# Optimization experiments

Hardware: AMD Instinct MI355X
Metric: run time of the kernel (lower is better)

## Reference

```python
import jax, jax.numpy as jnp
import numpy as np

SE = 128        # num_sensors
T = 256         # timesteps
D_OB = 4        # d_ob_emb
D_PE = 16
D_STATIC = 64
B = 128
N_HEADS = 4
D_FF = 128
N_TRAN = 2
N_PROP = 2
N_CLASSES = 2
D_FEAT = T * D_OB              # 1024, prop-layer feature dim
D_MODEL = SE * D_OB + D_PE     # 528, transformer d_model
D_FINAL = D_MODEL + SE * D_OB  # 1040, mlp input (with static emb)
LN_EPS = 1e-5
NEG_INF = -1e9


def _layernorm(x, g, b):
    m = jnp.mean(x, axis=-1, keepdims=True)
    v = jnp.mean(jnp.square(x - m), axis=-1, keepdims=True)
    return (x - m) * jax.lax.rsqrt(v + LN_EPS) * g + b


def setup_inputs() -> dict:
    key = jax.random.key(0)
    ks = iter(jax.random.split(key, 40))

    def g(shape, scale=0.02):
        return jax.random.normal(next(ks), shape, jnp.float32) * scale

    a = float(np.sqrt(6.0 / (1 + SE * D_OB)))  # glorot for R_u
    inp = {
        'src': jax.random.normal(next(ks), (T, B, 2 * SE), jnp.float32),
        'times': jax.random.uniform(next(ks), (T, B), jnp.float32) * T,
        'lengths': jax.random.randint(next(ks), (B,), 1, T + 1),
        'static': jax.random.normal(next(ks), (B, D_STATIC), jnp.float32),
        'R_u': jax.random.uniform(next(ks), (1, SE * D_OB), jnp.float32, -a, a),
        'static_W': g((SE * D_OB, D_STATIC)),
        'static_b': g((SE * D_OB,)),
        'p_Wq': g((N_PROP, D_FEAT, D_FEAT)),
        'p_Wk': g((N_PROP, D_FEAT, D_FEAT)),
        'p_Wv': g((N_PROP, D_FEAT, D_FEAT)),
        'p_bq': g((N_PROP, D_FEAT)),
        'p_bk': g((N_PROP, D_FEAT)),
        'p_bv': g((N_PROP, D_FEAT)),
        'p_Wskip': g((N_PROP, D_FEAT, D_FEAT)),
        'p_bskip': g((N_PROP, D_FEAT)),
        't_Wqkv': g((N_TRAN, 3 * D_MODEL, D_MODEL)),
        't_bqkv': g((N_TRAN, 3 * D_MODEL)),
        't_Wo': g((N_TRAN, D_MODEL, D_MODEL)),
        't_bo': g((N_TRAN, D_MODEL)),
        't_W1': g((N_TRAN, D_FF, D_MODEL)),
        't_b1': g((N_TRAN, D_FF)),
        't_W2': g((N_TRAN, D_MODEL, D_FF)),
        't_b2': g((N_TRAN, D_MODEL)),
        't_ln1g': jnp.ones((N_TRAN, D_MODEL), jnp.float32),
        't_ln1b': jnp.zeros((N_TRAN, D_MODEL), jnp.float32),
        't_ln2g': jnp.ones((N_TRAN, D_MODEL), jnp.float32),
        't_ln2b': jnp.zeros((N_TRAN, D_MODEL), jnp.float32),
        'mlp_W1': g((D_FINAL, D_FINAL)),
        'mlp_b1': g((D_FINAL,)),
        'mlp_W2': g((N_CLASSES, D_FINAL)),
        'mlp_b2': g((N_CLASSES,)),
    }
    return inp


def reference(src, times, lengths, static, R_u, static_W, static_b,
              p_Wq, p_Wk, p_Wv, p_bq, p_bk, p_bv, p_Wskip, p_bskip,
              t_Wqkv, t_bqkv, t_Wo, t_bo, t_W1, t_b1, t_W2, t_b2,
              t_ln1g, t_ln1b, t_ln2g, t_ln2b,
              mlp_W1, mlp_b1, mlp_W2, mlp_b2):
    # --- positional encoding (PositionalEncodingTF): sin/cos of times over timescales ---
    ts = jnp.asarray(float(T)) ** jnp.linspace(0.0, 1.0, D_PE // 2)
    st = times[..., None] / ts                       # (T,B,D_PE//2)
    pe = jnp.concatenate([jnp.sin(st), jnp.cos(st)], axis=-1)  # (T,B,D_PE)

    static_emb = static @ static_W.T + static_b      # (B, SE*D_OB)

    # --- per-sensor observation embedding ---
    x = src[:, :, :SE]
    x = jnp.repeat(x, D_OB, axis=-1)                 # (T,B,SE*D_OB)
    h = jax.nn.relu(x * R_u)                         # dropout = identity (eval)

    # --- diagonalized graphs: each batch element is a fully-connected Se-node graph.
    # The block-diagonal edge list over B*Se*Se edges is equivalent to dense
    # batched attention (B, Se, Se); we honor that structure densely. ---
    hg = h.reshape(T, B, SE, D_OB).transpose(1, 2, 0, 3).reshape(B, SE, D_FEAT)
    W = jnp.ones((B, SE, SE), h.dtype)               # edge weights [b, tgt, src], adj=ones
    scale = 1.0 / jnp.sqrt(jnp.asarray(D_FEAT, h.dtype))
    for l in range(N_PROP):
        q = hg @ p_Wq[l].T + p_bq[l]
        k = hg @ p_Wk[l].T + p_bk[l]
        v = hg @ p_Wv[l].T + p_bv[l]
        scores = jnp.einsum('bid,bjd->bij', q, k) * scale   # i=target, j=source
        alpha = jax.nn.softmax(scores, axis=-1)              # softmax over sources
        hg = jnp.einsum('bij,bjd->bid', alpha * W, v) + hg @ p_Wskip[l].T + p_bskip[l]
        W = alpha                                            # attn weights feed next layer

    out = hg.reshape(B, SE, T, D_OB).transpose(2, 0, 1, 3).reshape(T, B, SE * D_OB)
    out = jnp.concatenate([out, pe], axis=2)          # (T,B,D_MODEL)

    # --- transformer encoder (post-norm, relu FF, key_padding_mask) ---
    time_mask = jnp.arange(T)[None, :] >= lengths[:, None]   # (B,T) True = pad
    hd = D_MODEL // N_HEADS
    xx = out
    for l in range(N_TRAN):
        qkv = xx @ t_Wqkv[l].T + t_bqkv[l]            # (T,B,3*D_MODEL)
        q, k, v = jnp.split(qkv, 3, axis=-1)
        def _heads(z):
            return z.reshape(T, B, N_HEADS, hd).transpose(1, 2, 0, 3)  # (B,H,T,hd)
        qh, kh, vh = _heads(q), _heads(k), _heads(v)
        att = jnp.einsum('bhqd,bhkd->bhqk', qh, kh) / jnp.sqrt(jnp.asarray(hd, xx.dtype))
        att = jnp.where(time_mask[:, None, None, :], NEG_INF, att)
        att = jax.nn.softmax(att, axis=-1)
        o = jnp.einsum('bhqk,bhkd->bhqd', att, vh).transpose(2, 0, 1, 3).reshape(T, B, D_MODEL)
        o = o @ t_Wo[l].T + t_bo[l]
        xx = _layernorm(xx + o, t_ln1g[l], t_ln1b[l])
        ff = jax.nn.relu(xx @ t_W1[l].T + t_b1[l]) @ t_W2[l].T + t_b2[l]
        xx = _layernorm(xx + ff, t_ln2g[l], t_ln2b[l])

    # --- masked mean pooling over time, static concat, MLP head ---
    keep = (~time_mask).astype(xx.dtype).T[:, :, None]        # (T,B,1)
    pooled = jnp.sum(xx * keep, axis=0) / (lengths[:, None].astype(xx.dtype) + 1.0)
    pooled = jnp.concatenate([pooled, static_emb], axis=1)    # (B, D_FINAL)
    hid = jax.nn.relu(pooled @ mlp_W1.T + mlp_b1)
    return hid @ mlp_W2.T + mlp_b2                            # (B, N_CLASSES)
```

## Files before the change

### kernel.cpp

```cpp
#include <hip/hip_runtime.h>
#include <hip/hip_bf16.h>
#include <math.h>

#define SE_    128
#define T_     256
#define B_     128
#define NH_    4
#define HD_    132
#define D_MODEL_ 528
#define D_FINAL_ 1040
#define D_FF_  128

typedef __hip_bfloat16 bf16;
typedef __attribute__((ext_vector_type(8))) short bf16x8v;
typedef __attribute__((ext_vector_type(4))) float f32x4;

__device__ __forceinline__ float bfb(unsigned short u){
  union { float f; unsigned int i; } c; c.i = ((unsigned int)u) << 16; return c.f;
}
__device__ __forceinline__ unsigned short bfr(float x){
  unsigned u = __builtin_bit_cast(unsigned, x);
  unsigned r = (u + 0x7FFFu + ((u >> 16) & 1u)) >> 16;
  return (unsigned short)r;
}
__device__ __forceinline__ void split1(float x, short& h, short& l){
  const unsigned short hu = bfr(x);
  const unsigned short lu = bfr(x - bfb(hu));
  h = (short)hu; l = (short)lu;
}
__device__ __forceinline__ float prd(const short* p, long i, long lo){
  return bfb((unsigned short)p[i]) + bfb((unsigned short)p[i+lo]);
}
__device__ __forceinline__ float rdIn(const void* p, long i, int f32){
  return f32 ? ((const float*)p)[i] : __bfloat162float(((const bf16*)p)[i]);
}

__global__ void detect_k(const void* __restrict__ src, int* __restrict__ flag){
  const unsigned int* p = (const unsigned int*)src;
  int bad = 0;
  for (int i = threadIdx.x; i < 4096; i += 256){
    const unsigned int lo = p[i] & 0xFFFFu;
    const unsigned int e = (lo >> 7) & 0xFFu;
    if (e >= 0xC0u) bad++;
  }
  __shared__ int red[256];
  red[threadIdx.x] = bad; __syncthreads();
  for (int h = 128; h > 0; h >>= 1){
    if (threadIdx.x < h) red[threadIdx.x] += red[threadIdx.x+h];
    __syncthreads();
  }
  if (threadIdx.x == 0) *flag = (red[0] > 64) ? 1 : 0;
}

#define MAXE 40
struct CvtTab {
  const void* src[MAXE];
  long srcOff[MAXE];
  long dstOff[MAXE];
  int n[MAXE];
  int bstart[MAXE];
  int cnt;
};
__global__ void cvt_all(CvtTab tb, short* __restrict__ wts, long loW, const int* __restrict__ flag){
  const int b = blockIdx.x;
  int e = 0;
  for (int i = 1; i < tb.cnt; ++i) if (tb.bstart[i] <= b) e = i;
  const long i = (long)(b - tb.bstart[e])*256 + threadIdx.x;
  if (i >= tb.n[e]) return;
  const float v = rdIn(tb.src[e], tb.srcOff[e] + i, *flag);
  short h, l; split1(v, h, l);
  wts[tb.dstOff[e] + i] = h;
  wts[tb.dstOff[e] + i + loW] = l;
}

__device__ __forceinline__ int swz(int r){ return (r&3) ^ ((r>>2)&3); }

__device__ __forceinline__ void gllstage_pair(const short* __restrict__ g, long lo, long ld,
    int kb, int row_g0, int rmax, int tid, short* Lh, short* Ll){
  const int w = tid>>6, ln = tid&63;
  #pragma unroll
  for (int inst=0; inst<2; ++inst){
    const int r = (w*2+inst)*16 + (ln>>2);
    int gr = row_g0 + r; if (gr > rmax) gr = rmax;
    const int q = (ln&3) ^ (((ln>>2)&3) ^ ((ln>>4)&3));
    const short* p = g + (long)gr*ld + kb + q*8;
    short* dh = Lh + (w*2+inst)*512;
    short* dl = Ll + (w*2+inst)*512;
    __builtin_amdgcn_global_load_lds(
        (const __attribute__((address_space(1))) void*)p,
        (__attribute__((address_space(3))) void*)dh, 16, 0, 0);
    __builtin_amdgcn_global_load_lds(
        (const __attribute__((address_space(1))) void*)(p + lo),
        (__attribute__((address_space(3))) void*)dl, 16, 0, 0);
  }
}

__device__ __forceinline__ void regstage_pair(const short* __restrict__ g, long lo, long ld,
    int kb, int K, int row_g0, int rmax, int tid, short* Lh, short* Ll){
  const int r = tid>>1;
  int gr = row_g0 + r; if (gr > rmax) gr = rmax;
  const int s = swz(r);
  #pragma unroll
  for (int cq=0;cq<2;++cq){
    const int q = (tid&1)*2 + cq;
    const int k0 = kb + q*8;
    short bh[8], bl[8];
    const short* p = g + (long)gr*ld + k0;
    if (k0 + 8 <= K){
      *(int2*)(bh)   = *(const int2*)(p);      *(int2*)(bh+4) = *(const int2*)(p+4);
      *(int2*)(bl)   = *(const int2*)(p+lo);   *(int2*)(bl+4) = *(const int2*)(p+lo+4);
    } else {
      #pragma unroll
      for (int e=0;e<8;++e){
        const bool ok = (k0+e) < K;
        bh[e] = ok ? p[e] : (short)0;
        bl[e] = ok ? p[lo+e] : (short)0;
      }
    }
    const int c = q ^ s;
    *(int4*)&Lh[r*32 + c*8] = *(const int4*)bh;
    *(int4*)&Ll[r*32 + c*8] = *(const int4*)bl;
  }
}

__device__ __forceinline__ void regstage_f32(const float* __restrict__ g, long ld,
    int kb, int K, int row_g0, int rmax, int tid, short* Lh, short* Ll){
  const int r = tid>>1;
  int gr = row_g0 + r; if (gr > rmax) gr = rmax;
  const int s = swz(r);
  #pragma unroll
  for (int cq=0;cq<2;++cq){
    const int q = (tid&1)*2 + cq;
    const int k0 = kb + q*8;
    short bh[8], bl[8];
    const float* p = g + (long)gr*ld + k0;
    if (k0 + 8 <= K){
      float f[8];
      *(float4*)(f)   = *(const float4*)(p);
      *(float4*)(f+4) = *(const float4*)(p+4);
      #pragma unroll
      for (int e=0;e<8;++e) split1(f[e], bh[e], bl[e]);
    } else {
      #pragma unroll
      for (int e=0;e<8;++e){
        const float v = (k0+e < K) ? p[e] : 0.f;
        split1(v, bh[e], bl[e]);
      }
    }
    const int c = q ^ s;
    *(int4*)&Lh[r*32 + c*8] = *(const int4*)bh;
    *(int4*)&Ll[r*32 + c*8] = *(const int4*)bl;
  }
}

__device__ __forceinline__ void rd_frags(const short* Lh, const short* Ll,
                                         int wbase, int fr, int qlog,
                                         bf16x8v ah[4], bf16x8v al[4]){
  const int cs = (qlog ^ ((fr&3) ^ ((fr>>2)&3))) * 8;
  #pragma unroll
  for (int i=0;i<4;++i){
    const int r_ = wbase + i*16 + fr;
    ah[i] = *reinterpret_cast<const bf16x8v*>(&Lh[r_*32 + cs]);
    al[i] = *reinterpret_cast<const bf16x8v*>(&Ll[r_*32 + cs]);
  }
}

struct Route { short* C; long ldc; long lo; long sC; long sC2; int nEnd; int fl; };

template<bool SPLITA, bool GLL>
__global__ __launch_bounds__(256, 2) void gemm_s(
    const void* __restrict__ Ag, long loA,
    const short* __restrict__ Bg, long loB,
    const short* __restrict__ bias, long loBias,
    int M, int N, int K, long lda, long ldb,
    int nz1, long sA, long sB, long sA2, long sB2,
    int relu, int nroute, Route r0, Route r1, Route r2, float mult)
{
  __shared__ short As_h[128*32], As_l[128*32], Bs_h[128*32], Bs_l[128*32];
  const int tid = threadIdx.x;
  const int z1 = blockIdx.z % nz1, z2 = blockIdx.z / nz1;
  const int m0 = blockIdx.y*128, n0 = blockIdx.x*128;
  const void* A;
  if (SPLITA) A = (const void*)((const float*)Ag + z1*sA + z2*sA2);
  else        A = (const void*)((const short*)Ag + z1*sA + z2*sA2);
  const short* B = Bg + z1*sB + z2*sB2;
  short* Cb0 = r0.C + z1*r0.sC + z2*r0.sC2;
  short* Cb1 = (nroute > 1) ? (r1.C + z1*r1.sC + z2*r1.sC2) : nullptr;
  short* Cb2 = (nroute > 2) ? (r2.C + z1*r2.sC + z2*r2.sC2) : nullptr;

  const int lane = tid & 63, wv = tid >> 6;
  const int wm = (wv >> 1)*64, wn = (wv & 1)*64;
  const int fr = lane & 15, qlog = lane >> 4;

  f32x4 acc[4][4] = {};
  for (int kb = 0; kb < K; kb += 32){
    const bool tail = (kb + 32 > K);
    if (SPLITA) regstage_f32((const float*)A, lda, kb, K, m0, M-1, tid, As_h, As_l);
    else if (GLL && !tail) gllstage_pair((const short*)A, loA, lda, kb, m0, M-1, tid, As_h, As_l);
    else regstage_pair((const short*)A, loA, lda, kb, K, m0, M-1, tid, As_h, As_l);
    if (GLL && !tail) gllstage_pair(B, loB, ldb, kb, n0, N-1, tid, Bs_h, Bs_l);
    else regstage_pair(B, loB, ldb, kb, K, n0, N-1, tid, Bs_h, Bs_l);
    __syncthreads();

    bf16x8v ah[4], al[4], bh[4], bl[4];
    rd_frags(As_h, As_l, wm, fr, qlog, ah, al);
    rd_frags(Bs_h, Bs_l, wn, fr, qlog, bh, bl);
    #pragma unroll
    for (int j=0;j<4;++j)
      #pragma unroll
      for (int i=0;i<4;++i){
        acc[i][j] = __builtin_amdgcn_mfma_f32_16x16x32_bf16(ah[i], bh[j], acc[i][j], 0,0,0);
        acc[i][j] = __builtin_amdgcn_mfma_f32_16x16x32_bf16(ah[i], bl[j], acc[i][j], 0,0,0);
        acc[i][j] = __builtin_amdgcn_mfma_f32_16x16x32_bf16(al[i], bh[j], acc[i][j], 0,0,0);
      }
    __syncthreads();
  }

  const int cr = (lane >> 4)*4, cc = lane & 15;
  #pragma unroll
  for (int i=0;i<4;++i){
    #pragma unroll
    for (int j=0;j<4;++j){
      #pragma unroll
      for (int rr=0;rr<4;++rr){
        const int gm = m0 + wm + i*16 + cr + rr;
        const int gn = n0 + wn + j*16 + cc;
        if (gm < M && gn < N){
          float v = acc[i][j][rr] * mult;
          if (bias) v += prd(bias, gn, loBias);
          if (relu) v = fmaxf(v, 0.f);
          short* Cp; long ldc, lo; int fl, cn;
          if (nroute > 1 && gn >= r0.nEnd){
            if (nroute > 2 && gn >= r1.nEnd){ Cp=Cb2; ldc=r2.ldc; lo=r2.lo; fl=r2.fl; cn=gn-r1.nEnd; }
            else                            { Cp=Cb1; ldc=r1.ldc; lo=r1.lo; fl=r1.fl; cn=gn-r0.nEnd; }
          } else                            { Cp=Cb0; ldc=r0.ldc; lo=r0.lo; fl=r0.fl; cn=gn; }
          const long idx = (fl & 1) ? ((long)cn*ldc + gm) : ((long)gm*ldc + cn);
          if (fl & 2) v += prd(Cp, idx, lo);
          short h, l; split1(v, h, l);
          Cp[idx] = h; Cp[idx + lo] = l;
        }
      }
    }
  }
}

template<int NN, bool GLL>
__global__ __launch_bounds__(256, 2) void gemm_sm(
    const short* __restrict__ Ag, long loA, const short* __restrict__ Bg, long loB,
    int K, long lda, long ldb,
    int nz1, long sA, long sB, long sA2, long sB2,
    float* __restrict__ Sg, long sS, long sS2, int ldS,
    float mult, const int* __restrict__ lengths, int b0,
    const float* __restrict__ mulP, long sMul)
{
  __shared__ short As_h[128*32], As_l[128*32], Bs_h[128*32], Bs_l[128*32];
  const int tid = threadIdx.x;
  const int z1 = blockIdx.z % nz1, z2 = blockIdx.z / nz1;
  const int m0 = blockIdx.y*128;
  const short* A = Ag + z1*sA + z2*sA2;
  const short* B = Bg + z1*sB + z2*sB2;
  float* S = Sg + z1*sS + z2*sS2;

  const int lane = tid & 63, wv = tid >> 6;
  const int wm = (wv >> 1)*64, wn = (wv & 1)*64;
  const int fr = lane & 15, qlog = lane >> 4;
  const int cr = (lane >> 4)*4, cc = lane & 15;

  for (int nh = 0; nh < NN; nh += 128){
    f32x4 acc[4][4] = {};
    for (int kb = 0; kb < K; kb += 32){
      const bool tail = (kb + 32 > K);
      if (GLL && !tail){
        gllstage_pair(A, loA, lda, kb, m0, m0+127, tid, As_h, As_l);
        gllstage_pair(B, loB, ldb, kb, nh, nh+127, tid, Bs_h, Bs_l);
      } else {
        regstage_pair(A, loA, lda, kb, K, m0, m0+127, tid, As_h, As_l);
        regstage_pair(B, loB, ldb, kb, K, nh, nh+127, tid, Bs_h, Bs_l);
      }
      __syncthreads();
      bf16x8v ah[4], al[4], bh[4], bl[4];
      rd_frags(As_h, As_l, wm, fr, qlog, ah, al);
      rd_frags(Bs_h, Bs_l, wn, fr, qlog, bh, bl);
      #pragma unroll
      for (int j=0;j<4;++j)
        #pragma unroll
        for (int i=0;i<4;++i){
          acc[i][j] = __builtin_amdgcn_mfma_f32_16x16x32_bf16(ah[i], bh[j], acc[i][j], 0,0,0);
          acc[i][j] = __builtin_amdgcn_mfma_f32_16x16x32_bf16(ah[i], bl[j], acc[i][j], 0,0,0);
          acc[i][j] = __builtin_amdgcn_mfma_f32_16x16x32_bf16(al[i], bh[j], acc[i][j], 0,0,0);
        }
      __syncthreads();
    }
    #pragma unroll
    for (int i=0;i<4;++i)
      #pragma unroll
      for (int j=0;j<4;++j)
        #pragma unroll
        for (int rr=0;rr<4;++rr){
          const int gm = m0 + wm + i*16 + cr + rr;
          const int gn = nh + wn + j*16 + cc;
          S[(long)gm*ldS + gn] = acc[i][j][rr] * mult;
        }
  }
  __syncthreads();

  constexpr int CH = NN / 64;
  const int cbase = lane*CH;
  int lim = NN;
  if (lengths){ const int L = lengths[b0 + z1]; lim = (L < NN) ? L : NN; }

  float v[CH], vn[CH], mcur[CH], mnxt[CH];
  {
    float* row0 = S + (long)(m0 + wv*32)*ldS + cbase;
    #pragma unroll
    for (int e=0;e<CH;++e) v[e] = row0[e];
    if (mulP){
      const float* mr = mulP + z1*sMul + (long)(m0 + wv*32)*ldS + cbase;
      #pragma unroll
      for (int e=0;e<CH;++e) mcur[e] = mr[e];
    }
  }
  for (int i = 0; i < 32; ++i){
    if (i < 31){
      float* rn = S + (long)(m0 + wv*32 + i + 1)*ldS + cbase;
      #pragma unroll
      for (int e=0;e<CH;++e) vn[e] = rn[e];
      if (mulP){
        const float* mr = mulP + z1*sMul + (long)(m0 + wv*32 + i + 1)*ldS + cbase;
        #pragma unroll
        for (int e=0;e<CH;++e) mnxt[e] = mr[e];
      }
    }
    float mx = -3.0e38f;
    #pragma unroll
    for (int e=0;e<CH;++e) if (cbase+e < lim) mx = fmaxf(mx, v[e]);
    #pragma unroll
    for (int o=32;o>0;o>>=1) mx = fmaxf(mx, __shfl_xor(mx, o, 64));
    float sm = 0.f;
    #pragma unroll
    for (int e=0;e<CH;++e){
      v[e] = (cbase+e < lim) ? __expf(v[e] - mx) : 0.f;
      sm += v[e];
    }
    #pragma unroll
    for (int o=32;o>0;o>>=1) sm += __shfl_xor(sm, o, 64);
    const float inv = 1.f / sm;
    float* row = S + (long)(m0 + wv*32 + i)*ldS + cbase;
    if (mulP){
      #pragma unroll
      for (int e=0;e<CH;++e) row[e] = v[e]*inv*mcur[e];
    } else {
      #pragma unroll
      for (int e=0;e<CH;++e) row[e] = v[e]*inv;
    }
    #pragma unroll
    for (int e=0;e<CH;++e){ v[e] = vn[e]; mcur[e] = mnxt[e]; }
  }
}

__global__ void build_hg(const void* __restrict__ src, const short* __restrict__ Ru, long loW,
                         short* __restrict__ hg, long loH, const int* __restrict__ flag, int b0){
  const int t = blockIdx.x, bl = blockIdx.y, se = threadIdx.x;
  const int f32 = *flag;
  const float s = rdIn(src, ((long)t*B_ + (b0+bl))*(2*SE_) + se, f32);
  const long o = ((long)bl*SE_ + se)*1024 + t*4;
  #pragma unroll
  for (int j=0;j<4;++j){
    const float v = fmaxf(s * prd(Ru, se*4+j, loW), 0.f);
    short h, l; split1(v, h, l);
    hg[o+j] = h; hg[o+j+loH] = l;
  }
}

__global__ void build_xx(const short* __restrict__ hg, long loH,
                         const short* __restrict__ times, long loW,
                         short* __restrict__ xx, long loX, int b0, int G){
  const int blk = blockIdx.x;
  const int t = blk / G, bl = blk % G, b = b0 + bl;
  const int tid = threadIdx.x;
  const float tm = prd(times, (long)t*B_ + b, loW);
  for (int c = tid; c < D_MODEL_; c += 256){
    float v;
    if (c < SE_*4){
      v = prd(hg, ((long)bl*SE_ + (c>>2))*1024 + t*4 + (c&3), loH);
    } else {
      const int p = c - SE_*4;
      const int i = p & 7;
      const float ts = exp2f(8.0f * (float)i / 7.0f);
      const float st = tm / ts;
      v = (p < 8) ? sinf(st) : cosf(st);
    }
    short h, l; split1(v, h, l);
    const long o = ((long)t*B_ + b)*D_MODEL_ + c;
    xx[o] = h; xx[o+loX] = l;
  }
}

__device__ __forceinline__ void ln_body_p(short* px, long loX, const short* pr, long loR,
                                          const short* g, const short* bb, long loW, int tid){
  const float x0 = prd(px,tid,loX)     + prd(pr,tid,loR);
  const float x1 = prd(px,tid+256,loX) + prd(pr,tid+256,loR);
  const float x2 = (tid < 16) ? (prd(px,tid+512,loX) + prd(pr,tid+512,loR)) : 0.f;
  __shared__ float rs[256], rq[256];
  rs[tid] = x0 + x1 + x2;
  rq[tid] = x0*x0 + x1*x1 + x2*x2;
  __syncthreads();
  for (int h = 128; h > 0; h >>= 1){
    if (tid < h){ rs[tid] += rs[tid+h]; rq[tid] += rq[tid+h]; }
    __syncthreads();
  }
  const float mean = rs[0] * (1.0f/528.0f);
  const float var  = rq[0] * (1.0f/528.0f) - mean*mean;
  const float inv = rsqrtf(var + 1e-5f);
  short h, l;
  split1((x0-mean)*inv*prd(g,tid,loW) + prd(bb,tid,loW), h, l);
  px[tid] = h; px[tid+loX] = l;
  split1((x1-mean)*inv*prd(g,tid+256,loW) + prd(bb,tid+256,loW), h, l);
  px[tid+256] = h; px[tid+256+loX] = l;
  if (tid < 16){
    split1((x2-mean)*inv*prd(g,tid+512,loW) + prd(bb,tid+512,loW), h, l);
    px[tid+512] = h; px[tid+512+loX] = l;
  }
}

__global__ __launch_bounds__(256) void ln_res_attn(short* __restrict__ xx, long loX,
    const short* __restrict__ res, long loR,
    const short* __restrict__ g, const short* __restrict__ bb, long loW, int b0){
  const int z = blockIdx.x >> 8, t = blockIdx.x & 255;
  short* px = xx + ((long)t*B_ + b0 + z)*D_MODEL_;
  const short* pr = res + (long)blockIdx.x*D_MODEL_;
  ln_body_p(px, loX, pr, loR, g, bb, loW, threadIdx.x);
}

__global__ __launch_bounds__(256) void ln_res_rows(short* __restrict__ xx, long loX,
    const short* __restrict__ res, long loR,
    const short* __restrict__ g, const short* __restrict__ bb, long loW, int r0){
  short* px = xx + ((long)r0 + blockIdx.x)*D_MODEL_;
  const short* pr = res + (long)blockIdx.x*D_MODEL_;
  ln_body_p(px, loX, pr, loR, g, bb, loW, threadIdx.x);
}

__global__ void pool_k(const short* __restrict__ xx, long loX, const int* __restrict__ len,
                       short* __restrict__ pooled, long loP){
  const int b = blockIdx.y;
  const int c = blockIdx.x*256 + threadIdx.x;
  if (c >= D_MODEL_) return;
  const int L = len[b];
  float s = 0.f;
  for (int t = 0; t < L; ++t) s += prd(xx, ((long)t*B_ + b)*D_MODEL_ + c, loX);
  short h, l; split1(s / (float)(L + 1), h, l);
  pooled[(long)b*D_FINAL_ + c] = h;
  pooled[(long)b*D_FINAL_ + c + loP] = l;
}

__global__ void logits_k(const short* __restrict__ hid, long loH,
                         const short* __restrict__ W2, const short* __restrict__ b2, long loW,
                         void* __restrict__ out, const int* __restrict__ flag){
  const int z = blockIdx.x;
  const int b = z >> 1, c = z & 1;
  const int lane = threadIdx.x;
  float s = 0.f;
  for (int k = lane; k < D_FINAL_; k += 64)
    s += prd(hid, (long)b*D_FINAL_ + k, loH) * prd(W2, (long)c*D_FINAL_ + k, loW);
  #pragma unroll
  for (int o = 32; o > 0; o >>= 1) s += __shfl_down(s, o, 64);
  if (lane == 0){
    const float r = s + prd(b2, c, loW);
    if (*flag) ((float*)out)[z] = r;
    else       ((bf16*)out)[z] = __float2bfloat16(r);
  }
}

extern "C" void kernel_launch(void* const* d_in, const int* in_sizes, int n_in,
                              void* d_out, int out_size, void* d_ws, size_t ws_size,
                              hipStream_t stream) {
  const int* lengths = (const int*)d_in[2];
  char* ws = (char*)d_ws;
  const size_t KB = 1024;

  short* wtsH = (short*)ws;
  int* flag = (int*)(ws + 47500*KB);
  short* xxH = (short*)(ws + 48000*KB);
  const long loXX = 17301504;
  char* SC = ws + 115600*KB;

  short* hgA = (short*)(SC + 0*KB);      const long loHG = 2097152;
  short* hgB = (short*)(SC + 8192*KB);
  short* qkc = (short*)(SC + 16384*KB);  const long loQK1 = 4194304;
  short* VtS = (short*)(SC + 32768*KB);  const long loVT1 = 2097152;
  float* S0c = (float*)(SC + 40960*KB);
  float* S1c = (float*)(SC + 41984*KB);
  short* qkb = (short*)(SC + 0*KB);      const long loQK2 = 4325376;
  short* o_c = (short*)(SC + 0*KB);      const long loOC  = 2162688;
  short* pjb = (short*)(SC + 8448*KB);   const long loPJ  = 2162688;
  short* vtb = (short*)(SC + 16896*KB);  const long loVT2 = 2162688;
  float* att = (float*)(SC + 25344*KB);
  short* ff1 = (short*)(SC + 0*KB);      const long loFF  = 4194304;
  short* pj2 = (short*)(SC + 16896*KB);  const long loPJ2 = 4325376;
  short* pooled = (short*)(SC + 0*KB);   const long loPO  = 133120;
  short* hid    = (short*)(SC + 1024*KB);

  CvtTab tb; long cur = 0; int nb = 0; int e = 0;
  auto add = [&](int idx, long so, long n)->long{
    tb.src[e] = d_in[idx]; tb.srcOff[e] = so; tb.dstOff[e] = cur;
    tb.n[e] = (int)n; tb.bstart[e] = nb;
    nb += (int)((n + 255)/256); cur += n; e++;
    return cur - n;
  };
  const long oT  = add(1,0,32768);
  const long oSt = add(3,0,8192);
  const long oRu = add(4,0,512);
  const long oSW = add(5,0,32768);
  const long oSb = add(6,0,512);
  long oQKSV[2], oBQ[2];
  for (int l = 0; l < 2; ++l){
    oQKSV[l] = add(7, (long)l*1048576, 1048576);
    add(8,  (long)l*1048576, 1048576);
    add(13, (long)l*1048576, 1048576);
    add(9,  (long)l*1048576, 1048576);
  }
  for (int l = 0; l < 2; ++l){
    oBQ[l] = add(10, (long)l*1024, 1024);
    add(11, (long)l*1024, 1024);
    add(14, (long)l*1024, 1024);
    add(12, (long)l*1024, 1024);
  }
  const long oWqkv = add(15,0,1672704);
  const long obqkv = add(16,0,3168);
  const long oWo = add(17,0,557568);
  const long obo = add(18,0,1056);
  const long oW1 = add(19,0,135168);
  const long ob1 = add(20,0,256);
  const long oW2 = add(21,0,135168);
  const long ob2 = add(22,0,1056);
  const long og1 = add(23,0,1056);
  const long obb1 = add(24,0,1056);
  const long og2 = add(25,0,1056);
  const long obb2 = add(26,0,1056);
  const long oM1 = add(27,0,1081600);
  const long oM1b = add(28,0,1040);
  const long oM2 = add(29,0,2080);
  const long oM2b = add(30,0,2);
  tb.cnt = e;
  const long loW = (cur + 7) & ~7L;

  detect_k<<<1,256,0,stream>>>(d_in[0], flag);
  cvt_all<<<nb,256,0,stream>>>(tb, wtsH, loW, flag);

  const Route RZ{nullptr,0,0,0,0,0,0};

  const int G1 = 16;
  for (int b0 = 0; b0 < B_; b0 += G1){
    build_hg<<<dim3(T_, G1), 128, 0, stream>>>(d_in[0], wtsH+oRu, loW, hgA, loHG, flag, b0);
    short* curb = hgA; short* nxtb = hgB;
    for (int l = 0; l < 2; ++l){
      float* S = (l == 0) ? S0c : S1c;
      {
        Route q{qkc, 2048, loQK1, 0, 0, 2048, 0};
        Route s{nxtb, 1024, loHG, 0, 0, 3072, 0};
        Route v{VtS, 2048, loVT1, 0, 0, 4096, 1};
        gemm_s<false,true><<<dim3(32,16,1),256,0,stream>>>(
            curb, loHG, wtsH+oQKSV[l], loW, wtsH+oBQ[l], loW,
            2048, 4096, 1024, 1024, 1024,
            1, 0,0,0,0, 0, 3, q, s, v, 1.f);
      }
      gemm_sm<128,true><<<dim3(1,1,G1),256,0,stream>>>(
          qkc, loQK1, qkc+1024, loQK1,
          1024, 2048, 2048,
          G1, 262144, 262144, 0, 0,
          S, 16384, 0, 128,
          0.03125f, nullptr, 0,
          (l == 1) ? S0c : nullptr, 16384);
      {
        Route c{nxtb, 1024, loHG, 131072, 0, 1024, 2};
        gemm_s<true,true><<<dim3(8,1,G1),256,0,stream>>>(
            S, 0, VtS, loVT1, nullptr, 0,
            128, 1024, 128, 128, 2048,
            G1, 16384, 128, 0, 0, 0, 1, c, RZ, RZ, 1.f);
      }
      short* t_ = curb; curb = nxtb; nxtb = t_;
    }
    build_xx<<<T_*G1,256,0,stream>>>(curb, loHG, wtsH+oT, loW, xxH, loXX, b0, G1);
  }

  const float iscl = 1.0f / sqrtf((float)HD_);
  const int G2 = 16;
  for (int l = 0; l < 2; ++l){
    const long wqkv = oWqkv + (long)l*836352;
    const long bqkv = obqkv + (long)l*1584;
    for (int b0 = 0; b0 < B_; b0 += G2){
      {
        Route qk{qkb, 1056, loQK2, 270336, 0, 1056, 0};
        Route v{vtb, 256, loVT2, 135168, 0, 1584, 1};
        gemm_s<false,true><<<dim3(13,2,G2),256,0,stream>>>(
            xxH + (long)b0*D_MODEL_, loXX, wtsH+wqkv, loW, wtsH+bqkv, loW,
            256, 1584, 528, (long)B_*D_MODEL_, 528,
            G2, 528, 0, 0, 0, 0, 2, qk, v, RZ, 1.f);
      }
      gemm_sm<256,false><<<dim3(1,2,G2*NH_),256,0,stream>>>(
          qkb, loQK2, qkb+528, loQK2,
          132, 1056, 1056,
          G2, 270336, 270336, 132, 132,
          att, 262144, 65536, 256,
          iscl, lengths, b0, nullptr, 0);
      {
        Route c{o_c, 528, loOC, 135168, 132, HD_, 0};
        gemm_s<true,true><<<dim3(2,2,G2*NH_),256,0,stream>>>(
            att, 0, vtb, loVT2, nullptr, 0,
            256, HD_, 256, 256, 256,
            G2, 262144, 135168, 65536, 33792, 0, 1, c, RZ, RZ, 1.f);
      }
      {
        Route c{pjb, 528, loPJ, 135168, 0, 528, 0};
        gemm_s<false,true><<<dim3(5,2,G2),256,0,stream>>>(
            o_c, loOC, wtsH+oWo+(long)l*278784, loW, wtsH+obo+(long)l*528, loW,
            256, 528, 528, 528, 528,
            G2, 135168, 0, 0, 0, 0, 1, c, RZ, RZ, 1.f);
      }
      ln_res_attn<<<G2*256,256,0,stream>>>(xxH, loXX, pjb, loPJ,
          wtsH+og1+(long)l*528, wtsH+obb1+(long)l*528, loW, b0);
    }
    {
      Route c{ff1, 128, loFF, 0, 0, 128, 0};
      gemm_s<false,true><<<dim3(1,256,1),256,0,stream>>>(
          xxH, loXX, wtsH+oW1+(long)l*67584, loW, wtsH+ob1+(long)l*128, loW,
          32768, 128, 528, 528, 528,
          1, 0,0,0,0, 1, 1, c, RZ, RZ, 1.f);
    }
    for (int r0 = 0; r0 < 32768; r0 += 8192){
      Route c{pj2, 528, loPJ2, 0, 0, 528, 0};
      gemm_s<false,true><<<dim3(5,64,1),256,0,stream>>>(
          ff1 + (long)r0*128, loFF, wtsH+oW2+(long)l*67584, loW, wtsH+ob2+(long)l*528, loW,
          8192, 528, 128, 128, 128,
          1, 0,0,0,0, 0, 1, c, RZ, RZ, 1.f);
      ln_res_rows<<<8192,256,0,stream>>>(xxH, loXX, pj2, loPJ2,
          wtsH+og2+(long)l*528, wtsH+obb2+(long)l*528, loW, r0);
    }
  }

  pool_k<<<dim3(3,B_),256,0,stream>>>(xxH, loXX, lengths, pooled, loPO);
  {
    Route c{pooled + D_MODEL_, 1040, loPO, 0, 0, 512, 0};
    gemm_s<false,true><<<dim3(4,1,1),256,0,stream>>>(
        wtsH+oSt, loW, wtsH+oSW, loW, wtsH+oSb, loW,
        128, 512, 64, 64, 64,
        1, 0,0,0,0, 0, 1, c, RZ, RZ, 1.f);
  }
  {
    Route c{hid, 1040, loPO, 0, 0, 1040, 0};
    gemm_s<false,true><<<dim3(9,1,1),256,0,stream>>>(
        pooled, loPO, wtsH+oM1, loW, wtsH+oM1b, loW,
        128, 1040, 1040, 1040, 1040,
        1, 0,0,0,0, 1, 1, c, RZ, RZ, 1.f);
  }
  logits_k<<<B_*2,64,0,stream>>>(hid, loPO, wtsH+oM2, wtsH+oM2b, loW, d_out, flag);
}
```

Before: 7.114 ms.

## Double GEMM K-tile to 64 and vectorize weight conversion kernel

```diff
diff --git a/kernel.cpp b/kernel.cpp
--- a/kernel.cpp
+++ b/kernel.cpp
@@ -65,12 +65,35 @@
   const int b = blockIdx.x;
   int e = 0;
   for (int i = 1; i < tb.cnt; ++i) if (tb.bstart[i] <= b) e = i;
-  const long i = (long)(b - tb.bstart[e])*256 + threadIdx.x;
-  if (i >= tb.n[e]) return;
-  const float v = rdIn(tb.src[e], tb.srcOff[e] + i, *flag);
-  short h, l; split1(v, h, l);
-  wts[tb.dstOff[e] + i] = h;
-  wts[tb.dstOff[e] + i + loW] = l;
+  const long n = tb.n[e];
+  const long i0 = (long)(b - tb.bstart[e])*2048 + (long)threadIdx.x*8;
+  if (i0 >= n) return;
+  const int f32 = *flag;
+  if (i0 + 8 <= n){
+    short h8[8], l8[8];
+    if (f32){
+      const float* s = (const float*)tb.src[e] + tb.srcOff[e] + i0;
+      float f[8];
+      *(float4*)(f)   = *(const float4*)(s);
+      *(float4*)(f+4) = *(const float4*)(s+4);
+      #pragma unroll
+      for (int k=0;k<8;++k) split1(f[k], h8[k], l8[k]);
+    } else {
+      const short* s = (const short*)tb.src[e] + tb.srcOff[e] + i0;
+      *(int4*)h8 = *(const int4*)s;
+      #pragma unroll
+      for (int k=0;k<8;++k) l8[k] = 0;
+    }
+    *(int4*)(wts + tb.dstOff[e] + i0)       = *(const int4*)h8;
+    *(int4*)(wts + tb.dstOff[e] + i0 + loW) = *(const int4*)l8;
+  } else {
+    for (long k = i0; k < n; ++k){
+      const float v = rdIn(tb.src[e], tb.srcOff[e] + k, f32);
+      short h, l; split1(v, h, l);
+      wts[tb.dstOff[e] + k] = h;
+      wts[tb.dstOff[e] + k + loW] = l;
+    }
+  }
 }
 
 __device__ __forceinline__ int swz(int r){ return (r&3) ^ ((r>>2)&3); }
@@ -79,13 +102,16 @@
     int kb, int row_g0, int rmax, int tid, short* Lh, short* Ll){
   const int w = tid>>6, ln = tid&63;
   #pragma unroll
-  for (int inst=0; inst<2; ++inst){
-    const int r = (w*2+inst)*16 + (ln>>2);
+  for (int inst=0; inst<4; ++inst){
+    const int idx = w*4 + inst;
+    const int r = idx*8 + (ln>>3);
     int gr = row_g0 + r; if (gr > rmax) gr = rmax;
-    const int q = (ln&3) ^ (((ln>>2)&3) ^ ((ln>>4)&3));
+    const int c = ln & 7;
+    const int s = ((ln>>3)&3) ^ ((idx*2 + (ln>>5)) & 3);
+    const int q = (c & 4) | ((c & 3) ^ s);
     const short* p = g + (long)gr*ld + kb + q*8;
-    short* dh = Lh + (w*2+inst)*512;
-    short* dl = Ll + (w*2+inst)*512;
+    short* dh = Lh + idx*512;
+    short* dl = Ll + idx*512;
     __builtin_amdgcn_global_load_lds(
         (const __attribute__((address_space(1))) void*)p,
         (__attribute__((address_space(3))) void*)dh, 16, 0, 0);
@@ -101,8 +127,8 @@
   int gr = row_g0 + r; if (gr > rmax) gr = rmax;
   const int s = swz(r);
   #pragma unroll
-  for (int cq=0;cq<2;++cq){
-    const int q = (tid&1)*2 + cq;
+  for (int cq=0;cq<4;++cq){
+    const int q = (tid&1)*4 + cq;
     const int k0 = kb + q*8;
     short bh[8], bl[8];
     const short* p = g + (long)gr*ld + k0;
@@ -117,9 +143,9 @@
         bl[e] = ok ? p[lo+e] : (short)0;
       }
     }
-    const int c = q ^ s;
-    *(int4*)&Lh[r*32 + c*8] = *(const int4*)bh;
-    *(int4*)&Ll[r*32 + c*8] = *(const int4*)bl;
+    const int off = r*64 + (q>>2)*32 + ((q&3)^s)*8;
+    *(int4*)&Lh[off] = *(const int4*)bh;
+    *(int4*)&Ll[off] = *(const int4*)bl;
   }
 }
 
@@ -129,8 +155,8 @@
   int gr = row_g0 + r; if (gr > rmax) gr = rmax;
   const int s = swz(r);
   #pragma unroll
-  for (int cq=0;cq<2;++cq){
-    const int q = (tid&1)*2 + cq;
+  for (int cq=0;cq<4;++cq){
+    const int q = (tid&1)*4 + cq;
     const int k0 = kb + q*8;
     short bh[8], bl[8];
     const float* p = g + (long)gr*ld + k0;
@@ -147,21 +173,21 @@
         split1(v, bh[e], bl[e]);
       }
     }
-    const int c = q ^ s;
-    *(int4*)&Lh[r*32 + c*8] = *(const int4*)bh;
-    *(int4*)&Ll[r*32 + c*8] = *(const int4*)bl;
+    const int off = r*64 + (q>>2)*32 + ((q&3)^s)*8;
+    *(int4*)&Lh[off] = *(const int4*)bh;
+    *(int4*)&Ll[off] = *(const int4*)bl;
   }
 }
 
 __device__ __forceinline__ void rd_frags(const short* Lh, const short* Ll,
-                                         int wbase, int fr, int qlog,
+                                         int wbase, int fr, int qlog, int si,
                                          bf16x8v ah[4], bf16x8v al[4]){
-  const int cs = (qlog ^ ((fr&3) ^ ((fr>>2)&3))) * 8;
+  const int cs = si*32 + ((qlog ^ ((fr&3) ^ ((fr>>2)&3)))) * 8;
   #pragma unroll
   for (int i=0;i<4;++i){
     const int r_ = wbase + i*16 + fr;
-    ah[i] = *reinterpret_cast<const bf16x8v*>(&Lh[r_*32 + cs]);
-    al[i] = *reinterpret_cast<const bf16x8v*>(&Ll[r_*32 + cs]);
+    ah[i] = *reinterpret_cast<const bf16x8v*>(&Lh[r_*64 + cs]);
+    al[i] = *reinterpret_cast<const bf16x8v*>(&Ll[r_*64 + cs]);
   }
 }
 
@@ -176,7 +202,7 @@
     int nz1, long sA, long sB, long sA2, long sB2,
     int relu, int nroute, Route r0, Route r1, Route r2, float mult)
 {
-  __shared__ short As_h[128*32], As_l[128*32], Bs_h[128*32], Bs_l[128*32];
+  __shared__ short As_h[128*64], As_l[128*64], Bs_h[128*64], Bs_l[128*64];
   const int tid = threadIdx.x;
   const int z1 = blockIdx.z % nz1, z2 = blockIdx.z / nz1;
   const int m0 = blockIdx.y*128, n0 = blockIdx.x*128;
@@ -193,8 +219,8 @@
   const int fr = lane & 15, qlog = lane >> 4;
 
   f32x4 acc[4][4] = {};
-  for (int kb = 0; kb < K; kb += 32){
-    const bool tail = (kb + 32 > K);
+  for (int kb = 0; kb < K; kb += 64){
+    const bool tail = (kb + 64 > K);
     if (SPLITA) regstage_f32((const float*)A, lda, kb, K, m0, M-1, tid, As_h, As_l);
     else if (GLL && !tail) gllstage_pair((const short*)A, loA, lda, kb, m0, M-1, tid, As_h, As_l);
     else regstage_pair((const short*)A, loA, lda, kb, K, m0, M-1, tid, As_h, As_l);
@@ -202,17 +228,20 @@
     else regstage_pair(B, loB, ldb, kb, K, n0, N-1, tid, Bs_h, Bs_l);
     __syncthreads();
 
-    bf16x8v ah[4], al[4], bh[4], bl[4];
-    rd_frags(As_h, As_l, wm, fr, qlog, ah, al);
-    rd_frags(Bs_h, Bs_l, wn, fr, qlog, bh, bl);
-    #pragma unroll
-    for (int j=0;j<4;++j)
-      #pragma unroll
-      for (int i=0;i<4;++i){
-        acc[i][j] = __builtin_amdgcn_mfma_f32_16x16x32_bf16(ah[i], bh[j], acc[i][j], 0,0,0);
-        acc[i][j] = __builtin_amdgcn_mfma_f32_16x16x32_bf16(ah[i], bl[j], acc[i][j], 0,0,0);
-        acc[i][j] = __builtin_amdgcn_mfma_f32_16x16x32_bf16(al[i], bh[j], acc[i][j], 0,0,0);
-      }
+    #pragma unroll
+    for (int si=0; si<2; ++si){
+      bf16x8v ah[4], al[4], bh[4], bl[4];
+      rd_frags(As_h, As_l, wm, fr, qlog, si, ah, al);
+      rd_frags(Bs_h, Bs_l, wn, fr, qlog, si, bh, bl);
+      #pragma unroll
+      for (int j=0;j<4;++j)
+        #pragma unroll
+        for (int i=0;i<4;++i){
+          acc[i][j] = __builtin_amdgcn_mfma_f32_16x16x32_bf16(ah[i], bh[j], acc[i][j], 0,0,0);
+          acc[i][j] = __builtin_amdgcn_mfma_f32_16x16x32_bf16(ah[i], bl[j], acc[i][j], 0,0,0);
+          acc[i][j] = __builtin_amdgcn_mfma_f32_16x16x32_bf16(al[i], bh[j], acc[i][j], 0,0,0);
+        }
+    }
     __syncthreads();
   }
 
@@ -253,7 +282,7 @@
     float mult, const int* __restrict__ lengths, int b0,
     const float* __restrict__ mulP, long sMul)
 {
-  __shared__ short As_h[128*32], As_l[128*32], Bs_h[128*32], Bs_l[128*32];
+  __shared__ short As_h[128*64], As_l[128*64], Bs_h[128*64], Bs_l[128*64];
   const int tid = threadIdx.x;
   const int z1 = blockIdx.z % nz1, z2 = blockIdx.z / nz1;
   const int m0 = blockIdx.y*128;
@@ -268,8 +297,8 @@
 
   for (int nh = 0; nh < NN; nh += 128){
     f32x4 acc[4][4] = {};
-    for (int kb = 0; kb < K; kb += 32){
-      const bool tail = (kb + 32 > K);
+    for (int kb = 0; kb < K; kb += 64){
+      const bool tail = (kb + 64 > K);
       if (GLL && !tail){
         gllstage_pair(A, loA, lda, kb, m0, m0+127, tid, As_h, As_l);
         gllstage_pair(B, loB, ldb, kb, nh, nh+127, tid, Bs_h, Bs_l);
@@ -278,17 +307,20 @@
         regstage_pair(B, loB, ldb, kb, K, nh, nh+127, tid, Bs_h, Bs_l);
       }
       __syncthreads();
-      bf16x8v ah[4], al[4], bh[4], bl[4];
-      rd_frags(As_h, As_l, wm, fr, qlog, ah, al);
-      rd_frags(Bs_h, Bs_l, wn, fr, qlog, bh, bl);
-      #pragma unroll
-      for (int j=0;j<4;++j)
+      #pragma unroll
+      for (int si=0; si<2; ++si){
+        bf16x8v ah[4], al[4], bh[4], bl[4];
+        rd_frags(As_h, As_l, wm, fr, qlog, si, ah, al);
+        rd_frags(Bs_h, Bs_l, wn, fr, qlog, si, bh, bl);
         #pragma unroll
-        for (int i=0;i<4;++i){
-          acc[i][j] = __builtin_amdgcn_mfma_f32_16x16x32_bf16(ah[i], bh[j], acc[i][j], 0,0,0);
-          acc[i][j] = __builtin_amdgcn_mfma_f32_16x16x32_bf16(ah[i], bl[j], acc[i][j], 0,0,0);
-          acc[i][j] = __builtin_amdgcn_mfma_f32_16x16x32_bf16(al[i], bh[j], acc[i][j], 0,0,0);
-        }
+        for (int j=0;j<4;++j)
+          #pragma unroll
+          for (int i=0;i<4;++i){
+            acc[i][j] = __builtin_amdgcn_mfma_f32_16x16x32_bf16(ah[i], bh[j], acc[i][j], 0,0,0);
+            acc[i][j] = __builtin_amdgcn_mfma_f32_16x16x32_bf16(ah[i], bl[j], acc[i][j], 0,0,0);
+            acc[i][j] = __builtin_amdgcn_mfma_f32_16x16x32_bf16(al[i], bh[j], acc[i][j], 0,0,0);
+          }
+      }
       __syncthreads();
     }
     #pragma unroll
@@ -504,7 +536,7 @@
   auto add = [&](int idx, long so, long n)->long{
     tb.src[e] = d_in[idx]; tb.srcOff[e] = so; tb.dstOff[e] = cur;
     tb.n[e] = (int)n; tb.bstart[e] = nb;
-    nb += (int)((n + 255)/256); cur += n; e++;
+    nb += (int)((n + 2047)/2048); cur += n; e++;
     return cur - n;
   };
   const long oT  = add(1,0,32768);
```

New measurement: 6.713 ms. 1.06x faster.
